# Optimization experiments

Measured on AMD Instinct MI355X. Metric: run time of the kernel, lower is better.

## Reference

```python
import jax, jax.numpy as jnp
import numpy as np

N = 80000          # total nodes
F_IN = 16          # num_features
NUM_GRAPHS = 8
P = N // NUM_GRAPHS
EDGES_PER_GRAPH = 80000   # undirected samples per graph (~avg degree 16 after symmetrize)
OUT_DIM = 20000    # num_nodes (output classes)


def _graclus(src, dst, n, rng):
    """Greedy graclus matching (unweighted): visit nodes in random order, match with
    first unmatched neighbor. Cluster id = min(i, match[i]), relabeled consecutively."""
    perm = np.argsort(src, kind='stable')
    s, d = src[perm], dst[perm]
    starts = np.searchsorted(s, np.arange(n))
    ends = np.searchsorted(s, np.arange(n) + 1)
    match = np.full(n, -1, dtype=np.int64)
    for u in rng.permutation(n):
        if match[u] >= 0:
            continue
        match[u] = u
        for v in d[starts[u]:ends[u]]:
            if v != u and match[v] < 0:
                match[u] = v
                match[v] = u
                break
    rep = np.minimum(np.arange(n), match)
    _, cluster = np.unique(rep, return_inverse=True)
    return cluster.astype(np.int64)


def _pool_edges(src, dst, cluster, n1):
    """max_pool edge pooling: map endpoints to clusters, drop self-loops, coalesce."""
    cs, cd = cluster[src], cluster[dst]
    m = cs != cd
    key = np.unique(cs[m].astype(np.int64) * n1 + cd[m])
    return (key // n1).astype(np.int64), (key % n1).astype(np.int64)


def _glorot(k, shape):
    return jax.random.normal(k, shape, jnp.float32) * (2.0 / (shape[0] + shape[1])) ** 0.5


def setup_inputs() -> dict:
    rng = np.random.default_rng(0)
    srcs, dsts = [], []
    for g in range(NUM_GRAPHS):  # edges only within each graph block
        lo = g * P
        u = rng.integers(0, P, EDGES_PER_GRAPH)
        v = rng.integers(0, P, EDGES_PER_GRAPH)
        m = u != v
        u, v = u[m] + lo, v[m] + lo
        key = np.unique(np.minimum(u, v).astype(np.int64) * N + np.maximum(u, v))
        a, b = key // N, key % N
        srcs += [a, b]
        dsts += [b, a]
    src = np.concatenate(srcs).astype(np.int64)
    dst = np.concatenate(dsts).astype(np.int64)
    batch1 = (np.arange(N) // P).astype(np.int64)

    cluster1 = _graclus(src, dst, N, rng)
    n1 = int(cluster1.max()) + 1
    src2, dst2 = _pool_edges(src, dst, cluster1, n1)
    batch2 = np.zeros(n1, np.int64)
    batch2[cluster1] = batch1
    cluster2 = _graclus(src2, dst2, n1, rng)
    n2 = int(cluster2.max()) + 1
    batch3 = np.zeros(n2, np.int64)
    batch3[cluster2] = batch2

    ks = jax.random.split(jax.random.key(0), 12)
    return dict(
        x=jax.random.normal(ks[0], (N, F_IN), jnp.float32),
        W0a=_glorot(ks[1], (F_IN, 32)), W1a=_glorot(ks[2], (F_IN, 32)),
        b1=jnp.zeros((32,), jnp.float32),
        W0b=_glorot(ks[3], (32, 64)), W1b=_glorot(ks[4], (32, 64)),
        b2=jnp.zeros((64,), jnp.float32),
        fcw1=_glorot(ks[5], (64, 128)), fcb1=jnp.zeros((128,), jnp.float32),
        fcw2=_glorot(ks[6], (128, OUT_DIM)), fcb2=jnp.zeros((OUT_DIM,), jnp.float32),
        edge_index1=jnp.asarray(np.stack([src, dst])),
        cluster1=jnp.asarray(cluster1),
        edge_index2=jnp.asarray(np.stack([src2, dst2])),
        cluster2=jnp.asarray(cluster2),
        batch3=jnp.asarray(batch3),
        n1=n1, n2=n2, n_graphs=NUM_GRAPHS,
    )


def _cheb_relu(x, edge_index, W0, W1, b, n):
    """PyG ChebConv K=2, sym norm, lambda_max=2: out = x@W0 + (L~ x)@W1 + b with
    L~ = L - I = -D^{-1/2} A D^{-1/2}; then ReLU."""
    s, d = edge_index[0], edge_index[1]
    deg = jax.ops.segment_sum(jnp.ones(s.shape[0], x.dtype), d, num_segments=n)
    dinv = jnp.where(deg > 0, deg ** -0.5, 0.0)
    w = -(dinv[s] * dinv[d])                       # [E]
    tx1 = jax.ops.segment_sum(w[:, None] * x[s], d, num_segments=n)  # L~ x
    return jax.nn.relu(x @ W0 + tx1 @ W1 + b)


def reference(x, W0a, W1a, b1, W0b, W1b, b2, fcw1, fcb1, fcw2, fcb2,
              edge_index1, cluster1, edge_index2, cluster2, batch3,
              n1, n2, n_graphs):
    h = _cheb_relu(x, edge_index1, W0a, W1a, b1, x.shape[0])     # [N,32]
    hp = jax.ops.segment_max(h, cluster1, num_segments=n1)        # max_pool -> [n1,32]
    h2 = _cheb_relu(hp, edge_index2, W0b, W1b, b2, n1)            # [n1,64]
    h3 = jax.ops.segment_max(h2, cluster2, num_segments=n2)       # max_pool_x -> [n2,64]
    sums = jax.ops.segment_sum(h3, batch3, num_segments=n_graphs)
    cnt = jax.ops.segment_sum(jnp.ones(h3.shape[0], h3.dtype), batch3, num_segments=n_graphs)
    g = sums / cnt[:, None]                                       # global_mean_pool [G,64]
    g = jax.nn.relu(g @ fcw1 + fcb1)                              # dropout is eval-mode identity
    return g @ fcw2 + fcb2                                        # [G, OUT_DIM]
```

## Files before the change

### kernel.cpp

```cpp
#include <hip/hip_runtime.h>

static inline int idiv(int a, int b) { return (a + b - 1) / b; }

__device__ __forceinline__ int swz8(int bid, int nb) {
    int q = nb >> 3, r = nb & 7;
    int x = bid & 7, c = bid >> 3;
    return (x < r ? x * (q + 1) : r * (q + 1) + (x - r) * q) + c;
}

__global__ void k_zero(float4* __restrict__ p, long n4) {
    long t = (long)blockIdx.x * blockDim.x + threadIdx.x;
    long stride = (long)gridDim.x * blockDim.x;
    for (; t < n4; t += stride) p[t] = make_float4(0.f, 0.f, 0.f, 0.f);
}

__global__ void k_prep1(const int* __restrict__ src, const int* __restrict__ dst,
                        int* __restrict__ ust, int* __restrict__ uen,
                        int* __restrict__ cntS, int E) {
    int e = blockIdx.x * blockDim.x + threadIdx.x;
    if (e >= E) return;
    int s = src[e], d = dst[e];
    if (s >= d) return;
    atomicAdd(&cntS[d], 1);
    bool prevup = false; int ps = -1;
    if (e > 0) { ps = src[e - 1]; prevup = (ps < dst[e - 1]); }
    if (e == 0 || !prevup || ps != s) ust[s] = e;
    bool nextup = false; int ns = -1;
    if (e + 1 < E) { ns = src[e + 1]; nextup = (ns < dst[e + 1]); }
    if (e + 1 == E || !nextup || ns != s) uen[s] = e + 1;
}

__global__ void k_bounds2(const int* __restrict__ src, int* __restrict__ rs,
                          int* __restrict__ re, int E) {
    int e = blockIdx.x * blockDim.x + threadIdx.x;
    if (e >= E) return;
    int s = src[e];
    if (e == 0 || src[e - 1] != s) rs[s] = e;
    if (e + 1 == E || src[e + 1] != s) re[s] = e + 1;
}

__global__ void k_dinv2(const int* __restrict__ rs, const int* __restrict__ re,
                        float* __restrict__ dinv, int n) {
    int t = blockIdx.x * blockDim.x + threadIdx.x;
    if (t < n) {
        int deg = re[t] - rs[t];
        dinv[t] = (deg > 0) ? rsqrtf((float)deg) : 0.0f;
    }
}

__global__ void k_members(const int* __restrict__ cl, int* __restrict__ mcnt,
                          int* __restrict__ mem, int n) {
    int t = blockIdx.x * blockDim.x + threadIdx.x;
    if (t >= n) return;
    int c = cl[t];
    int slot = atomicAdd(&mcnt[c], 1);
    if (slot < 2) mem[2 * c + slot] = t;
}

__global__ void k_scan_blk(const int* __restrict__ cnt, int* __restrict__ offs,
                           int* __restrict__ blksum, int n) {
    __shared__ int ts[256];
    int blk = blockIdx.x;
    int tid = threadIdx.x;
    int i0 = blk * 1024 + tid * 4;
    int a0 = 0, a1 = 0, a2 = 0, a3 = 0;
    if (i0 + 3 < n) {
        int4 v = *(const int4*)&cnt[i0];
        a0 = v.x; a1 = v.y; a2 = v.z; a3 = v.w;
    } else {
        if (i0 + 0 < n) a0 = cnt[i0 + 0];
        if (i0 + 1 < n) a1 = cnt[i0 + 1];
        if (i0 + 2 < n) a2 = cnt[i0 + 2];
    }
    int tsum = a0 + a1 + a2 + a3;
    ts[tid] = tsum;
    __syncthreads();
    for (int off = 1; off < 256; off <<= 1) {
        int v = (tid >= off) ? ts[tid - off] : 0;
        __syncthreads();
        ts[tid] += v;
        __syncthreads();
    }
    int ex = ts[tid] - tsum;
    if (tid == 255) blksum[blk] = ts[255];
    int p0 = ex, p1 = ex + a0, p2 = p1 + a1, p3 = p2 + a2;
    if (i0 + 3 < n) {
        *(int4*)&offs[i0] = make_int4(p0, p1, p2, p3);
    } else {
        if (i0 + 0 < n) offs[i0 + 0] = p0;
        if (i0 + 1 < n) offs[i0 + 1] = p1;
        if (i0 + 2 < n) offs[i0 + 2] = p2;
    }
}

__global__ void k_scan_tot(int* __restrict__ blksum, int nblk) {
    __shared__ int s[1024];
    int tid = threadIdx.x;
    int v = (tid < nblk) ? blksum[tid] : 0;
    s[tid] = v;
    __syncthreads();
    for (int off = 1; off < 1024; off <<= 1) {
        int t = (tid >= off) ? s[tid - off] : 0;
        __syncthreads();
        s[tid] += t;
        __syncthreads();
    }
    if (tid < nblk) blksum[tid] = s[tid] - v;
}

__global__ void k_scan_add_dinv(int* __restrict__ offs, int* __restrict__ cursor,
                                const int* __restrict__ blksum, const int* __restrict__ cntS,
                                const int* __restrict__ ust, const int* __restrict__ uen,
                                float* __restrict__ dinv, int n) {
    int t = blockIdx.x * blockDim.x + threadIdx.x;
    if (t < n) {
        int v = offs[t] + blksum[t >> 10];
        offs[t] = v;
        cursor[t] = v;
        int deg = cntS[t] + uen[t] - ust[t];
        dinv[t] = (deg > 0) ? rsqrtf((float)deg) : 0.0f;
    }
}

__global__ void k_fillS(const int* __restrict__ src, const int* __restrict__ dst,
                        int* __restrict__ cursor, int* __restrict__ csr, int E) {
    int e = blockIdx.x * blockDim.x + threadIdx.x;
    if (e >= E) return;
    int s = src[e], d = dst[e];
    if (s < d) {
        int pos = atomicAdd(&cursor[d], 1);
        csr[pos] = s;
    }
}

__global__ void k_gather1v(const int* __restrict__ ust, const int* __restrict__ uen,
                           const int* __restrict__ dst1, const int* __restrict__ offsS,
                           const int* __restrict__ cntS, const int* __restrict__ csrS,
                           const float* __restrict__ dinv, const float* __restrict__ xin,
                           float* __restrict__ tx, int n) {
    int vb = swz8(blockIdx.x, gridDim.x);
    int t = vb * blockDim.x + threadIdx.x;
    int d = t >> 2, fo = (t & 3) << 2;
    if (d >= n) return;
    float ax = 0.f, ay = 0.f, az = 0.f, aw = 0.f;
    int e = ust[d], e1 = uen[d];
    for (; e + 1 < e1; e += 2) {
        int s0 = dst1[e], s1 = dst1[e + 1];
        float w0 = dinv[s0], w1 = dinv[s1];
        float4 v0 = *(const float4*)&xin[((long)s0 << 4) + fo];
        float4 v1 = *(const float4*)&xin[((long)s1 << 4) + fo];
        ax += w0 * v0.x + w1 * v1.x;
        ay += w0 * v0.y + w1 * v1.y;
        az += w0 * v0.z + w1 * v1.z;
        aw += w0 * v0.w + w1 * v1.w;
    }
    for (; e < e1; e++) {
        int s = dst1[e];
        float w = dinv[s];
        float4 v = *(const float4*)&xin[((long)s << 4) + fo];
        ax += w * v.x; ay += w * v.y; az += w * v.z; aw += w * v.w;
    }
    int i = offsS[d], i1 = i + cntS[d];
    for (; i + 1 < i1; i += 2) {
        int s0 = csrS[i], s1 = csrS[i + 1];
        float w0 = dinv[s0], w1 = dinv[s1];
        float4 v0 = *(const float4*)&xin[((long)s0 << 4) + fo];
        float4 v1 = *(const float4*)&xin[((long)s1 << 4) + fo];
        ax += w0 * v0.x + w1 * v1.x;
        ay += w0 * v0.y + w1 * v1.y;
        az += w0 * v0.z + w1 * v1.z;
        aw += w0 * v0.w + w1 * v1.w;
    }
    for (; i < i1; i++) {
        int s = csrS[i];
        float w = dinv[s];
        float4 v = *(const float4*)&xin[((long)s << 4) + fo];
        ax += w * v.x; ay += w * v.y; az += w * v.z; aw += w * v.w;
    }
    float wd = -dinv[d];
    *(float4*)&tx[((long)d << 4) + fo] = make_float4(wd * ax, wd * ay, wd * az, wd * aw);
}

__global__ void k_gather2v(const int* __restrict__ rs, const int* __restrict__ re,
                           const int* __restrict__ dst2, const float* __restrict__ dinv,
                           const float* __restrict__ xin, float* __restrict__ tx, int n) {
    int vb = swz8(blockIdx.x, gridDim.x);
    int t = vb * blockDim.x + threadIdx.x;
    int d = t >> 3, fo = (t & 7) << 2;
    if (d >= n) return;
    float ax = 0.f, ay = 0.f, az = 0.f, aw = 0.f;
    int j = rs[d], j1 = re[d];
    for (; j + 1 < j1; j += 2) {
        int s0 = dst2[j], s1 = dst2[j + 1];
        float w0 = dinv[s0], w1 = dinv[s1];
        float4 v0 = *(const float4*)&xin[((long)s0 << 5) + fo];
        float4 v1 = *(const float4*)&xin[((long)s1 << 5) + fo];
        ax += w0 * v0.x + w1 * v1.x;
        ay += w0 * v0.y + w1 * v1.y;
        az += w0 * v0.z + w1 * v1.z;
        aw += w0 * v0.w + w1 * v1.w;
    }
    for (; j < j1; j++) {
        int s = dst2[j];
        float w = dinv[s];
        float4 v = *(const float4*)&xin[((long)s << 5) + fo];
        ax += w * v.x; ay += w * v.y; az += w * v.z; aw += w * v.w;
    }
    float wd = -dinv[d];
    *(float4*)&tx[((long)d << 5) + fo] = make_float4(wd * ax, wd * ay, wd * az, wd * aw);
}

__global__ void k_cheb1(const float* __restrict__ x, const float* __restrict__ tx,
                        const float* __restrict__ W0, const float* __restrict__ W1,
                        const float* __restrict__ b, float* __restrict__ h, int N) {
    int t = blockIdx.x * blockDim.x + threadIdx.x;
    int n = t >> 3, jj = (t & 7) << 2;
    if (n >= N) return;
    const float4* xr = (const float4*)(x + (long)n * 16);
    const float4* tr = (const float4*)(tx + (long)n * 16);
    float4 bv = *(const float4*)(b + jj);
    float a0 = bv.x, a1 = bv.y, a2 = bv.z, a3 = bv.w;
#pragma unroll
    for (int k4 = 0; k4 < 4; k4++) {
        float4 xv = xr[k4];
        float4 tv = tr[k4];
        float xs[4] = {xv.x, xv.y, xv.z, xv.w};
        float ts[4] = {tv.x, tv.y, tv.z, tv.w};
#pragma unroll
        for (int c = 0; c < 4; c++) {
            int k = k4 * 4 + c;
            float4 w0 = *(const float4*)(W0 + k * 32 + jj);
            float4 w1 = *(const float4*)(W1 + k * 32 + jj);
            a0 += xs[c] * w0.x + ts[c] * w1.x;
            a1 += xs[c] * w0.y + ts[c] * w1.y;
            a2 += xs[c] * w0.z + ts[c] * w1.z;
            a3 += xs[c] * w0.w + ts[c] * w1.w;
        }
    }
    *(float4*)(h + ((long)n << 5) + jj) =
        make_float4(fmaxf(a0, 0.f), fmaxf(a1, 0.f), fmaxf(a2, 0.f), fmaxf(a3, 0.f));
}

__global__ void k_pool1(const int* __restrict__ mcnt, const int* __restrict__ mem,
                        const float* __restrict__ h, float* __restrict__ hp, int n1) {
    int t = blockIdx.x * blockDim.x + threadIdx.x;
    int c = t >> 3, fo = (t & 7) << 2;
    if (c >= n1) return;
    int m0 = mem[2 * c];
    float4 v = *(const float4*)&h[((long)m0 << 5) + fo];
    if (mcnt[c] > 1) {
        int m1 = mem[2 * c + 1];
        float4 u = *(const float4*)&h[((long)m1 << 5) + fo];
        v.x = fmaxf(v.x, u.x); v.y = fmaxf(v.y, u.y);
        v.z = fmaxf(v.z, u.z); v.w = fmaxf(v.w, u.w);
    }
    *(float4*)&hp[((long)c << 5) + fo] = v;
}

__global__ void k_cheb2(const float* __restrict__ xp, const float* __restrict__ tx,
                        const float* __restrict__ W0, const float* __restrict__ W1,
                        const float* __restrict__ b, float* __restrict__ h2, int n1) {
    int t = blockIdx.x * blockDim.x + threadIdx.x;
    int n = t >> 4, jj = (t & 15) << 2;
    if (n >= n1) return;
    const float4* xr = (const float4*)(xp + (long)n * 32);
    const float4* tr = (const float4*)(tx + (long)n * 32);
    float4 bv = *(const float4*)(b + jj);
    float a0 = bv.x, a1 = bv.y, a2 = bv.z, a3 = bv.w;
#pragma unroll
    for (int k4 = 0; k4 < 8; k4++) {
        float4 xv = xr[k4];
        float4 tv = tr[k4];
        float xs[4] = {xv.x, xv.y, xv.z, xv.w};
        float ts[4] = {tv.x, tv.y, tv.z, tv.w};
#pragma unroll
        for (int c = 0; c < 4; c++) {
            int k = k4 * 4 + c;
            float4 w0 = *(const float4*)(W0 + k * 64 + jj);
            float4 w1 = *(const float4*)(W1 + k * 64 + jj);
            a0 += xs[c] * w0.x + ts[c] * w1.x;
            a1 += xs[c] * w0.y + ts[c] * w1.y;
            a2 += xs[c] * w0.z + ts[c] * w1.z;
            a3 += xs[c] * w0.w + ts[c] * w1.w;
        }
    }
    *(float4*)(h2 + ((long)n << 6) + jj) =
        make_float4(fmaxf(a0, 0.f), fmaxf(a1, 0.f), fmaxf(a2, 0.f), fmaxf(a3, 0.f));
}

__global__ void k_gsum2(const float* __restrict__ h2, const int* __restrict__ mcnt,
                        const int* __restrict__ mem, const int* __restrict__ batch,
                        float* __restrict__ gsum, float* __restrict__ gcnt, int n2) {
    __shared__ float s[8 * 64];
    __shared__ float sc[8];
    for (int i = threadIdx.x; i < 512; i += blockDim.x) s[i] = 0.0f;
    if (threadIdx.x < 8) sc[threadIdx.x] = 0.0f;
    __syncthreads();
    long total = (long)n2 * 64;
    long stride = (long)gridDim.x * blockDim.x;
    for (long t = (long)blockIdx.x * blockDim.x + threadIdx.x; t < total; t += stride) {
        int c = (int)(t >> 6), f = (int)(t & 63);
        int m0 = mem[2 * c];
        float v = h2[((long)m0 << 6) + f];
        if (mcnt[c] > 1) {
            int m1 = mem[2 * c + 1];
            v = fmaxf(v, h2[((long)m1 << 6) + f]);
        }
        int g = batch[c];
        atomicAdd(&s[g * 64 + f], v);
        if (f == 0) atomicAdd(&sc[g], 1.0f);
    }
    __syncthreads();
    for (int i = threadIdx.x; i < 512; i += blockDim.x) atomicAdd(&gsum[i], s[i]);
    if (threadIdx.x < 8) atomicAdd(&gcnt[threadIdx.x], sc[threadIdx.x]);
}

__global__ void k_fc1(const float* __restrict__ gsum, const float* __restrict__ gcnt,
                      const float* __restrict__ fcw1, const float* __restrict__ fcb1,
                      float* __restrict__ g1) {
    __shared__ float sg[8 * 64];
    int tid = threadIdx.x;
    if (tid < 512) {
        float c = gcnt[tid >> 6];
        sg[tid] = (c > 0.0f) ? gsum[tid] / c : 0.0f;
    }
    __syncthreads();
    int gi = tid >> 7, j = tid & 127;
    float acc = fcb1[j];
#pragma unroll 8
    for (int k = 0; k < 64; k++) acc += sg[gi * 64 + k] * fcw1[k * 128 + j];
    g1[tid] = fmaxf(acc, 0.0f);
}

__global__ void k_fc2(const float* __restrict__ g1, const float* __restrict__ fcw2,
                      const float* __restrict__ fcb2, float* __restrict__ out, int OUT) {
    __shared__ float sg[8 * 128];
    for (int i = threadIdx.x; i < 1024; i += blockDim.x) sg[i] = g1[i];
    __syncthreads();
    int o = blockIdx.x * blockDim.x + threadIdx.x;
    if (o >= OUT) return;
    float bias = fcb2[o];
    float acc[8];
#pragma unroll
    for (int gi = 0; gi < 8; gi++) acc[gi] = bias;
    for (int k = 0; k < 128; k++) {
        float w = fcw2[(long)k * OUT + o];
#pragma unroll
        for (int gi = 0; gi < 8; gi++) acc[gi] += sg[gi * 128 + k] * w;
    }
#pragma unroll
    for (int gi = 0; gi < 8; gi++) out[(long)gi * OUT + o] = acc[gi];
}

extern "C" void kernel_launch(void* const* d_in, const int* in_sizes, int n_in,
                              void* d_out, int out_size, void* d_ws, size_t ws_size,
                              hipStream_t stream) {
    const float* x    = (const float*)d_in[0];
    const float* W0a  = (const float*)d_in[1];
    const float* W1a  = (const float*)d_in[2];
    const float* b1   = (const float*)d_in[3];
    const float* W0b  = (const float*)d_in[4];
    const float* W1b  = (const float*)d_in[5];
    const float* b2   = (const float*)d_in[6];
    const float* fcw1 = (const float*)d_in[7];
    const float* fcb1 = (const float*)d_in[8];
    const float* fcw2 = (const float*)d_in[9];
    const float* fcb2 = (const float*)d_in[10];
    const int* ei1    = (const int*)d_in[11];
    const int* cl1    = (const int*)d_in[12];
    const int* ei2    = (const int*)d_in[13];
    const int* cl2    = (const int*)d_in[14];
    const int* b3     = (const int*)d_in[15];

    const int N  = in_sizes[12];
    const int E1 = in_sizes[11] / 2;
    const int E2 = in_sizes[13] / 2;
    const int n1 = in_sizes[14];
    const int n2 = in_sizes[15];
    const int G  = 8;
    const int OUT = out_size / G;

    const int nmax = (N > n1) ? N : n1;
    long hElems = (long)N * 32;
    if ((long)n1 * 64 > hElems) hElems = (long)n1 * 64;

    auto rnd = [](size_t b) { return (b + 255) & ~(size_t)255; };
    size_t cntB  = rnd((size_t)N * 4);
    size_t ustB  = rnd((size_t)N * 4);
    size_t uenB  = rnd((size_t)N * 4);
    size_t rs2B  = rnd((size_t)n1 * 4);
    size_t re2B  = rnd((size_t)n1 * 4);
    size_t mc1B  = rnd((size_t)n1 * 4);
    size_t mc2B  = rnd((size_t)n2 * 4);
    size_t smlB  = rnd((512 + 8 + 1024) * 4);
    size_t offB  = rnd((size_t)N * 4);
    size_t curB  = rnd((size_t)N * 4);
    size_t csrB  = rnd((size_t)(E1 / 2 + 64) * 4);
    size_t dinvB = rnd((size_t)nmax * 4);
    size_t blkB  = rnd((size_t)1024 * 4);
    size_t mem1B = rnd((size_t)n1 * 2 * 4);
    size_t mem2B = rnd((size_t)n2 * 2 * 4);
    size_t hpB   = rnd((size_t)n1 * 32 * 4);
    size_t txB   = rnd((size_t)(((long)N * 16 > (long)n1 * 32) ? (long)N * 16 : (long)n1 * 32) * 4);

    char* base = (char*)d_ws;
    char* p = base;
    int*   cntS   = (int*)p;           p += cntB;
    int*   ust    = (int*)p;           p += ustB;
    int*   uen    = (int*)p;           p += uenB;
    int*   rs2    = (int*)p;           p += rs2B;
    int*   re2    = (int*)p;           p += re2B;
    int*   mcnt1  = (int*)p;           p += mc1B;
    int*   mcnt2  = (int*)p;           p += mc2B;
    float* gsum   = (float*)p;         p += smlB;
    float* gcnt   = gsum + 512;
    float* g1     = gcnt + 8;
    size_t zeroB  = (size_t)(p - base);
    int*   offsS  = (int*)p;           p += offB;
    int*   cursorS= (int*)p;           p += curB;
    int*   csrS   = (int*)p;           p += csrB;
    float* dinv   = (float*)p;         p += dinvB;
    int*   blksum = (int*)p;           p += blkB;
    int*   mem1   = (int*)p;           p += mem1B;
    int*   mem2   = (int*)p;           p += mem2B;
    float* hp     = (float*)p;         p += hpB;
    float* txA    = (float*)p;         p += txB;
    float* hbuf   = (float*)p;
    (void)ws_size;

    dim3 B(256);
    {
        long n4 = (long)(zeroB / 16);
        int g = idiv((int)((n4 < 1048576) ? n4 : 1048576), 256);
        if (g < 1) g = 1;
        if (g > 4096) g = 4096;
        k_zero<<<g, B, 0, stream>>>((float4*)base, n4);
    }

    {
        int nblk = idiv(N, 1024);
        k_prep1<<<idiv(E1, 256), B, 0, stream>>>(ei1, ei1 + E1, ust, uen, cntS, E1);
        k_members<<<idiv(N, 256), B, 0, stream>>>(cl1, mcnt1, mem1, N);
        k_scan_blk<<<nblk, B, 0, stream>>>(cntS, offsS, blksum, N);
        k_scan_tot<<<1, 1024, 0, stream>>>(blksum, nblk);
        k_scan_add_dinv<<<idiv(N, 256), B, 0, stream>>>(offsS, cursorS, blksum, cntS, ust, uen,
                                                        dinv, N);
        k_fillS<<<idiv(E1, 256), B, 0, stream>>>(ei1, ei1 + E1, cursorS, csrS, E1);
        k_gather1v<<<idiv(N * 4, 256), B, 0, stream>>>(ust, uen, ei1 + E1, offsS, cntS, csrS,
                                                       dinv, x, txA, N);
        k_cheb1<<<idiv(N * 8, 256), B, 0, stream>>>(x, txA, W0a, W1a, b1, hbuf, N);
        k_pool1<<<idiv(n1 * 8, 256), B, 0, stream>>>(mcnt1, mem1, hbuf, hp, n1);
    }

    {
        k_bounds2<<<idiv(E2, 256), B, 0, stream>>>(ei2, rs2, re2, E2);
        k_members<<<idiv(n1, 256), B, 0, stream>>>(cl2, mcnt2, mem2, n1);
        k_dinv2<<<idiv(n1, 256), B, 0, stream>>>(rs2, re2, dinv, n1);
        k_gather2v<<<idiv(n1 * 8, 256), B, 0, stream>>>(rs2, re2, ei2 + E2, dinv, hp, txA, n1);
        k_cheb2<<<idiv(n1 * 16, 256), B, 0, stream>>>(hp, txA, W0b, W1b, b2, hbuf, n1);
    }

    int gb = idiv(n2 * 64, 256);
    if (gb > 256) gb = 256;
    k_gsum2<<<gb, B, 0, stream>>>(hbuf, mcnt2, mem2, b3, gsum, gcnt, n2);
    k_fc1<<<1, 1024, 0, stream>>>(gsum, gcnt, fcw1, fcb1, g1);
    k_fc2<<<idiv(OUT, 256), B, 0, stream>>>(g1, fcw2, fcb2, (float*)d_out, OUT);
}
```

Measured before the change: 231.1 us.

## Fuse max-pooling into Cheb layers via atomicMax and merge FC layers

```diff
diff --git a/kernel.cpp b/kernel.cpp
--- a/kernel.cpp
+++ b/kernel.cpp
@@ -48,15 +48,6 @@
     }
 }
 
-__global__ void k_members(const int* __restrict__ cl, int* __restrict__ mcnt,
-                          int* __restrict__ mem, int n) {
-    int t = blockIdx.x * blockDim.x + threadIdx.x;
-    if (t >= n) return;
-    int c = cl[t];
-    int slot = atomicAdd(&mcnt[c], 1);
-    if (slot < 2) mem[2 * c + slot] = t;
-}
-
 __global__ void k_scan_blk(const int* __restrict__ cnt, int* __restrict__ offs,
                            int* __restrict__ blksum, int n) {
     __shared__ int ts[256];
@@ -140,42 +131,36 @@
                            float* __restrict__ tx, int n) {
     int vb = swz8(blockIdx.x, gridDim.x);
     int t = vb * blockDim.x + threadIdx.x;
-    int d = t >> 2, fo = (t & 3) << 2;
+    int d = t >> 2, ln = t & 3, fo = ln << 2;
     if (d >= n) return;
     float ax = 0.f, ay = 0.f, az = 0.f, aw = 0.f;
-    int e = ust[d], e1 = uen[d];
-    for (; e + 1 < e1; e += 2) {
-        int s0 = dst1[e], s1 = dst1[e + 1];
-        float w0 = dinv[s0], w1 = dinv[s1];
-        float4 v0 = *(const float4*)&xin[((long)s0 << 4) + fo];
-        float4 v1 = *(const float4*)&xin[((long)s1 << 4) + fo];
-        ax += w0 * v0.x + w1 * v1.x;
-        ay += w0 * v0.y + w1 * v1.y;
-        az += w0 * v0.z + w1 * v1.z;
-        aw += w0 * v0.w + w1 * v1.w;
-    }
-    for (; e < e1; e++) {
-        int s = dst1[e];
-        float w = dinv[s];
-        float4 v = *(const float4*)&xin[((long)s << 4) + fo];
-        ax += w * v.x; ay += w * v.y; az += w * v.z; aw += w * v.w;
-    }
-    int i = offsS[d], i1 = i + cntS[d];
-    for (; i + 1 < i1; i += 2) {
-        int s0 = csrS[i], s1 = csrS[i + 1];
-        float w0 = dinv[s0], w1 = dinv[s1];
-        float4 v0 = *(const float4*)&xin[((long)s0 << 4) + fo];
-        float4 v1 = *(const float4*)&xin[((long)s1 << 4) + fo];
-        ax += w0 * v0.x + w1 * v1.x;
-        ay += w0 * v0.y + w1 * v1.y;
-        az += w0 * v0.z + w1 * v1.z;
-        aw += w0 * v0.w + w1 * v1.w;
-    }
-    for (; i < i1; i++) {
-        int s = csrS[i];
-        float w = dinv[s];
-        float4 v = *(const float4*)&xin[((long)s << 4) + fo];
-        ax += w * v.x; ay += w * v.y; az += w * v.z; aw += w * v.w;
+    int e0 = ust[d], e1 = uen[d];
+    for (int j = e0; j < e1; j += 4) {
+        int myj = j + ln;
+        int s = 0; float w = 0.f;
+        if (myj < e1) { s = dst1[myj]; w = dinv[s]; }
+#pragma unroll
+        for (int k = 0; k < 4; k++) {
+            if (j + k >= e1) break;
+            int sk = __shfl(s, k, 4);
+            float wk = __shfl(w, k, 4);
+            float4 v = *(const float4*)&xin[((long)sk << 4) + fo];
+            ax += wk * v.x; ay += wk * v.y; az += wk * v.z; aw += wk * v.w;
+        }
+    }
+    int i0 = offsS[d], i1 = i0 + cntS[d];
+    for (int j = i0; j < i1; j += 4) {
+        int myj = j + ln;
+        int s = 0; float w = 0.f;
+        if (myj < i1) { s = csrS[myj]; w = dinv[s]; }
+#pragma unroll
+        for (int k = 0; k < 4; k++) {
+            if (j + k >= i1) break;
+            int sk = __shfl(s, k, 4);
+            float wk = __shfl(w, k, 4);
+            float4 v = *(const float4*)&xin[((long)sk << 4) + fo];
+            ax += wk * v.x; ay += wk * v.y; az += wk * v.z; aw += wk * v.w;
+        }
     }
     float wd = -dinv[d];
     *(float4*)&tx[((long)d << 4) + fo] = make_float4(wd * ax, wd * ay, wd * az, wd * aw);
@@ -186,33 +171,31 @@
                            const float* __restrict__ xin, float* __restrict__ tx, int n) {
     int vb = swz8(blockIdx.x, gridDim.x);
     int t = vb * blockDim.x + threadIdx.x;
-    int d = t >> 3, fo = (t & 7) << 2;
+    int d = t >> 3, ln = t & 7, fo = ln << 2;
     if (d >= n) return;
     float ax = 0.f, ay = 0.f, az = 0.f, aw = 0.f;
-    int j = rs[d], j1 = re[d];
-    for (; j + 1 < j1; j += 2) {
-        int s0 = dst2[j], s1 = dst2[j + 1];
-        float w0 = dinv[s0], w1 = dinv[s1];
-        float4 v0 = *(const float4*)&xin[((long)s0 << 5) + fo];
-        float4 v1 = *(const float4*)&xin[((long)s1 << 5) + fo];
-        ax += w0 * v0.x + w1 * v1.x;
-        ay += w0 * v0.y + w1 * v1.y;
-        az += w0 * v0.z + w1 * v1.z;
-        aw += w0 * v0.w + w1 * v1.w;
-    }
-    for (; j < j1; j++) {
-        int s = dst2[j];
-        float w = dinv[s];
-        float4 v = *(const float4*)&xin[((long)s << 5) + fo];
-        ax += w * v.x; ay += w * v.y; az += w * v.z; aw += w * v.w;
+    int j0 = rs[d], j1 = re[d];
+    for (int j = j0; j < j1; j += 8) {
+        int myj = j + ln;
+        int s = 0; float w = 0.f;
+        if (myj < j1) { s = dst2[myj]; w = dinv[s]; }
+#pragma unroll
+        for (int k = 0; k < 8; k++) {
+            if (j + k >= j1) break;
+            int sk = __shfl(s, k, 8);
+            float wk = __shfl(w, k, 8);
+            float4 v = *(const float4*)&xin[((long)sk << 5) + fo];
+            ax += wk * v.x; ay += wk * v.y; az += wk * v.z; aw += wk * v.w;
+        }
     }
     float wd = -dinv[d];
     *(float4*)&tx[((long)d << 5) + fo] = make_float4(wd * ax, wd * ay, wd * az, wd * aw);
 }
 
-__global__ void k_cheb1(const float* __restrict__ x, const float* __restrict__ tx,
-                        const float* __restrict__ W0, const float* __restrict__ W1,
-                        const float* __restrict__ b, float* __restrict__ h, int N) {
+__global__ void k_cheb1_max(const float* __restrict__ x, const float* __restrict__ tx,
+                            const float* __restrict__ W0, const float* __restrict__ W1,
+                            const float* __restrict__ b, const int* __restrict__ cl,
+                            float* __restrict__ hp, int N) {
     int t = blockIdx.x * blockDim.x + threadIdx.x;
     int n = t >> 3, jj = (t & 7) << 2;
     if (n >= N) return;
@@ -237,29 +220,17 @@
             a3 += xs[c] * w0.w + ts[c] * w1.w;
         }
     }
-    *(float4*)(h + ((long)n << 5) + jj) =
-        make_float4(fmaxf(a0, 0.f), fmaxf(a1, 0.f), fmaxf(a2, 0.f), fmaxf(a3, 0.f));
-}
-
-__global__ void k_pool1(const int* __restrict__ mcnt, const int* __restrict__ mem,
-                        const float* __restrict__ h, float* __restrict__ hp, int n1) {
-    int t = blockIdx.x * blockDim.x + threadIdx.x;
-    int c = t >> 3, fo = (t & 7) << 2;
-    if (c >= n1) return;
-    int m0 = mem[2 * c];
-    float4 v = *(const float4*)&h[((long)m0 << 5) + fo];
-    if (mcnt[c] > 1) {
-        int m1 = mem[2 * c + 1];
-        float4 u = *(const float4*)&h[((long)m1 << 5) + fo];
-        v.x = fmaxf(v.x, u.x); v.y = fmaxf(v.y, u.y);
-        v.z = fmaxf(v.z, u.z); v.w = fmaxf(v.w, u.w);
-    }
-    *(float4*)&hp[((long)c << 5) + fo] = v;
-}
-
-__global__ void k_cheb2(const float* __restrict__ xp, const float* __restrict__ tx,
-                        const float* __restrict__ W0, const float* __restrict__ W1,
-                        const float* __restrict__ b, float* __restrict__ h2, int n1) {
+    long o = ((long)cl[n] << 5) + jj;
+    atomicMax((int*)&hp[o + 0], __float_as_int(fmaxf(a0, 0.f)));
+    atomicMax((int*)&hp[o + 1], __float_as_int(fmaxf(a1, 0.f)));
+    atomicMax((int*)&hp[o + 2], __float_as_int(fmaxf(a2, 0.f)));
+    atomicMax((int*)&hp[o + 3], __float_as_int(fmaxf(a3, 0.f)));
+}
+
+__global__ void k_cheb2_max(const float* __restrict__ xp, const float* __restrict__ tx,
+                            const float* __restrict__ W0, const float* __restrict__ W1,
+                            const float* __restrict__ b, const int* __restrict__ cl,
+                            float* __restrict__ h3, int n1) {
     int t = blockIdx.x * blockDim.x + threadIdx.x;
     int n = t >> 4, jj = (t & 15) << 2;
     if (n >= n1) return;
@@ -284,60 +255,58 @@
             a3 += xs[c] * w0.w + ts[c] * w1.w;
         }
     }
-    *(float4*)(h2 + ((long)n << 6) + jj) =
-        make_float4(fmaxf(a0, 0.f), fmaxf(a1, 0.f), fmaxf(a2, 0.f), fmaxf(a3, 0.f));
-}
-
-__global__ void k_gsum2(const float* __restrict__ h2, const int* __restrict__ mcnt,
-                        const int* __restrict__ mem, const int* __restrict__ batch,
+    long o = ((long)cl[n] << 6) + jj;
+    atomicMax((int*)&h3[o + 0], __float_as_int(fmaxf(a0, 0.f)));
+    atomicMax((int*)&h3[o + 1], __float_as_int(fmaxf(a1, 0.f)));
+    atomicMax((int*)&h3[o + 2], __float_as_int(fmaxf(a2, 0.f)));
+    atomicMax((int*)&h3[o + 3], __float_as_int(fmaxf(a3, 0.f)));
+}
+
+__global__ void k_gsum3(const float* __restrict__ h3, const int* __restrict__ batch,
                         float* __restrict__ gsum, float* __restrict__ gcnt, int n2) {
     __shared__ float s[8 * 64];
     __shared__ float sc[8];
     for (int i = threadIdx.x; i < 512; i += blockDim.x) s[i] = 0.0f;
     if (threadIdx.x < 8) sc[threadIdx.x] = 0.0f;
     __syncthreads();
-    long total = (long)n2 * 64;
+    long total = (long)n2 * 16;
     long stride = (long)gridDim.x * blockDim.x;
     for (long t = (long)blockIdx.x * blockDim.x + threadIdx.x; t < total; t += stride) {
-        int c = (int)(t >> 6), f = (int)(t & 63);
-        int m0 = mem[2 * c];
-        float v = h2[((long)m0 << 6) + f];
-        if (mcnt[c] > 1) {
-            int m1 = mem[2 * c + 1];
-            v = fmaxf(v, h2[((long)m1 << 6) + f]);
-        }
+        int c = (int)(t >> 4), f4 = (int)(t & 15);
+        float4 v = *(const float4*)&h3[((long)c << 6) + (f4 << 2)];
         int g = batch[c];
-        atomicAdd(&s[g * 64 + f], v);
-        if (f == 0) atomicAdd(&sc[g], 1.0f);
+        atomicAdd(&s[g * 64 + f4 * 4 + 0], v.x);
+        atomicAdd(&s[g * 64 + f4 * 4 + 1], v.y);
+        atomicAdd(&s[g * 64 + f4 * 4 + 2], v.z);
+        atomicAdd(&s[g * 64 + f4 * 4 + 3], v.w);
+        if (f4 == 0) atomicAdd(&sc[g], 1.0f);
     }
     __syncthreads();
     for (int i = threadIdx.x; i < 512; i += blockDim.x) atomicAdd(&gsum[i], s[i]);
     if (threadIdx.x < 8) atomicAdd(&gcnt[threadIdx.x], sc[threadIdx.x]);
 }
 
-__global__ void k_fc1(const float* __restrict__ gsum, const float* __restrict__ gcnt,
-                      const float* __restrict__ fcw1, const float* __restrict__ fcb1,
-                      float* __restrict__ g1) {
-    __shared__ float sg[8 * 64];
+__global__ void k_fc12(const float* __restrict__ gsum, const float* __restrict__ gcnt,
+                       const float* __restrict__ fcw1, const float* __restrict__ fcb1,
+                       const float* __restrict__ fcw2, const float* __restrict__ fcb2,
+                       float* __restrict__ out, int OUT) {
+    __shared__ float sm[8 * 64];
+    __shared__ float sg[8 * 128];
     int tid = threadIdx.x;
-    if (tid < 512) {
-        float c = gcnt[tid >> 6];
-        sg[tid] = (c > 0.0f) ? gsum[tid] / c : 0.0f;
-    }
-    __syncthreads();
-    int gi = tid >> 7, j = tid & 127;
-    float acc = fcb1[j];
+    for (int i = tid; i < 512; i += blockDim.x) {
+        float c = gcnt[i >> 6];
+        sm[i] = (c > 0.0f) ? gsum[i] / c : 0.0f;
+    }
+    __syncthreads();
+    for (int e = tid; e < 1024; e += blockDim.x) {
+        int gi = e >> 7, j = e & 127;
+        float acc = fcb1[j];
 #pragma unroll 8
-    for (int k = 0; k < 64; k++) acc += sg[gi * 64 + k] * fcw1[k * 128 + j];
-    g1[tid] = fmaxf(acc, 0.0f);
-}
-
-__global__ void k_fc2(const float* __restrict__ g1, const float* __restrict__ fcw2,
-                      const float* __restrict__ fcb2, float* __restrict__ out, int OUT) {
-    __shared__ float sg[8 * 128];
-    for (int i = threadIdx.x; i < 1024; i += blockDim.x) sg[i] = g1[i];
-    __syncthreads();
-    int o = blockIdx.x * blockDim.x + threadIdx.x;
+        for (int k = 0; k < 64; k++) acc += sm[gi * 64 + k] * fcw1[k * 128 + j];
+        sg[e] = fmaxf(acc, 0.0f);
+    }
+    __syncthreads();
+    int o = blockIdx.x * blockDim.x + tid;
     if (o >= OUT) return;
     float bias = fcb2[o];
     float acc[8];
@@ -381,8 +350,6 @@
     const int OUT = out_size / G;
 
     const int nmax = (N > n1) ? N : n1;
-    long hElems = (long)N * 32;
-    if ((long)n1 * 64 > hElems) hElems = (long)n1 * 64;
 
     auto rnd = [](size_t b) { return (b + 255) & ~(size_t)255; };
     size_t cntB  = rnd((size_t)N * 4);
@@ -390,18 +357,14 @@
     size_t uenB  = rnd((size_t)N * 4);
     size_t rs2B  = rnd((size_t)n1 * 4);
     size_t re2B  = rnd((size_t)n1 * 4);
-    size_t mc1B  = rnd((size_t)n1 * 4);
-    size_t mc2B  = rnd((size_t)n2 * 4);
-    size_t smlB  = rnd((512 + 8 + 1024) * 4);
+    size_t hpB   = rnd((size_t)n1 * 32 * 4);
+    size_t h3B   = rnd((size_t)n2 * 64 * 4);
+    size_t smlB  = rnd((512 + 8) * 4);
     size_t offB  = rnd((size_t)N * 4);
     size_t curB  = rnd((size_t)N * 4);
     size_t csrB  = rnd((size_t)(E1 / 2 + 64) * 4);
     size_t dinvB = rnd((size_t)nmax * 4);
     size_t blkB  = rnd((size_t)1024 * 4);
-    size_t mem1B = rnd((size_t)n1 * 2 * 4);
-    size_t mem2B = rnd((size_t)n2 * 2 * 4);
-    size_t hpB   = rnd((size_t)n1 * 32 * 4);
-    size_t txB   = rnd((size_t)(((long)N * 16 > (long)n1 * 32) ? (long)N * 16 : (long)n1 * 32) * 4);
 
     char* base = (char*)d_ws;
     char* p = base;
@@ -410,22 +373,17 @@
     int*   uen    = (int*)p;           p += uenB;
     int*   rs2    = (int*)p;           p += rs2B;
     int*   re2    = (int*)p;           p += re2B;
-    int*   mcnt1  = (int*)p;           p += mc1B;
-    int*   mcnt2  = (int*)p;           p += mc2B;
+    float* hp     = (float*)p;         p += hpB;
+    float* h3     = (float*)p;         p += h3B;
     float* gsum   = (float*)p;         p += smlB;
     float* gcnt   = gsum + 512;
-    float* g1     = gcnt + 8;
     size_t zeroB  = (size_t)(p - base);
     int*   offsS  = (int*)p;           p += offB;
     int*   cursorS= (int*)p;           p += curB;
     int*   csrS   = (int*)p;           p += csrB;
     float* dinv   = (float*)p;         p += dinvB;
     int*   blksum = (int*)p;           p += blkB;
-    int*   mem1   = (int*)p;           p += mem1B;
-    int*   mem2   = (int*)p;           p += mem2B;
-    float* hp     = (float*)p;         p += hpB;
-    float* txA    = (float*)p;         p += txB;
-    float* hbuf   = (float*)p;
+    float* txA    = (float*)p;
     (void)ws_size;
 
     dim3 B(256);
@@ -440,7 +398,6 @@
     {
         int nblk = idiv(N, 1024);
         k_prep1<<<idiv(E1, 256), B, 0, stream>>>(ei1, ei1 + E1, ust, uen, cntS, E1);
-        k_members<<<idiv(N, 256), B, 0, stream>>>(cl1, mcnt1, mem1, N);
         k_scan_blk<<<nblk, B, 0, stream>>>(cntS, offsS, blksum, N);
         k_scan_tot<<<1, 1024, 0, stream>>>(blksum, nblk);
         k_scan_add_dinv<<<idiv(N, 256), B, 0, stream>>>(offsS, cursorS, blksum, cntS, ust, uen,
@@ -448,21 +405,19 @@
         k_fillS<<<idiv(E1, 256), B, 0, stream>>>(ei1, ei1 + E1, cursorS, csrS, E1);
         k_gather1v<<<idiv(N * 4, 256), B, 0, stream>>>(ust, uen, ei1 + E1, offsS, cntS, csrS,
                                                        dinv, x, txA, N);
-        k_cheb1<<<idiv(N * 8, 256), B, 0, stream>>>(x, txA, W0a, W1a, b1, hbuf, N);
-        k_pool1<<<idiv(n1 * 8, 256), B, 0, stream>>>(mcnt1, mem1, hbuf, hp, n1);
+        k_cheb1_max<<<idiv(N * 8, 256), B, 0, stream>>>(x, txA, W0a, W1a, b1, cl1, hp, N);
     }
 
     {
         k_bounds2<<<idiv(E2, 256), B, 0, stream>>>(ei2, rs2, re2, E2);
-        k_members<<<idiv(n1, 256), B, 0, stream>>>(cl2, mcnt2, mem2, n1);
         k_dinv2<<<idiv(n1, 256), B, 0, stream>>>(rs2, re2, dinv, n1);
         k_gather2v<<<idiv(n1 * 8, 256), B, 0, stream>>>(rs2, re2, ei2 + E2, dinv, hp, txA, n1);
-        k_cheb2<<<idiv(n1 * 16, 256), B, 0, stream>>>(hp, txA, W0b, W1b, b2, hbuf, n1);
-    }
-
-    int gb = idiv(n2 * 64, 256);
+        k_cheb2_max<<<idiv(n1 * 16, 256), B, 0, stream>>>(hp, txA, W0b, W1b, b2, cl2, h3, n1);
+    }
+
+    int gb = idiv(n2 * 16, 256);
     if (gb > 256) gb = 256;
-    k_gsum2<<<gb, B, 0, stream>>>(hbuf, mcnt2, mem2, b3, gsum, gcnt, n2);
-    k_fc1<<<1, 1024, 0, stream>>>(gsum, gcnt, fcw1, fcb1, g1);
-    k_fc2<<<idiv(OUT, 256), B, 0, stream>>>(g1, fcw2, fcb2, (float*)d_out, OUT);
-}
+    k_gsum3<<<gb, B, 0, stream>>>(h3, b3, gsum, gcnt, n2);
+    k_fc12<<<idiv(OUT, 256), B, 0, stream>>>(gsum, gcnt, fcw1, fcb1, fcw2, fcb2,
+                                             (float*)d_out, OUT);
+}
```

Result: slower. 255.1 us (+10.4%).
